# Kernel tuning notes

Hardware: AMD Instinct MI355X
Metric: run time of the kernel (lower is better)

The kernel has to match this reference:

```python
import jax, jax.numpy as jnp
import numpy as np

NUM_CLASSES = 80
ANCHORS = np.array([[10,13],[16,30],[33,23],[30,61],[62,45],[59,119],[116,90],[156,198],[373,326]], np.float32)
MASK = [[0,1,2],[3,4,5],[6,7,8]]
STRIDES = [8, 16, 32]
MAX_OUT = 100      # max_output_size_per_class == max_total_size
IOU_THR = 0.45
SCORE_THR = 0.25
NMS_TOPK = 128     # per-class candidate pre-selection for greedy NMS (>= MAX_OUT)


def setup_inputs() -> dict:
    key = jax.random.key(0)
    k1, k2, k3 = jax.random.split(key, 3)
    B = 16
    C = 3 * (NUM_CLASSES + 5)  # 255
    return {
        'p3': jax.random.normal(k1, (B, 80, 80, C), jnp.float32),
        'p4': jax.random.normal(k2, (B, 40, 40, C), jnp.float32),
        'p5': jax.random.normal(k3, (B, 20, 20, C), jnp.float32),
    }


def _decode(logits, anchors, stride):
    # logits: [B,H,W,3*(nc+5)] -> boxes [B,H*W*3,4] (x1y1x2y2), obj [B,M], cls [B,M,nc]
    B, H, W, _ = logits.shape
    A = anchors.shape[0]
    x = logits.reshape(B, H, W, A, NUM_CLASSES + 5)
    xy = jax.nn.sigmoid(x[..., :2])
    wh_logit = x[..., 2:4]
    obj = jax.nn.sigmoid(x[..., 4])
    cls = jax.nn.sigmoid(x[..., 5:])
    gx, gy = jnp.meshgrid(jnp.arange(W, dtype=x.dtype), jnp.arange(H, dtype=x.dtype))
    grid = jnp.stack([gx, gy], axis=-1)[:, :, None, :]  # [H,W,1,2]
    ctr = (xy + grid) * stride
    wh = jnp.exp(wh_logit) * anchors  # [B,H,W,A,2]
    box = jnp.concatenate([ctr - wh / 2.0, ctr + wh / 2.0], axis=-1)
    return box.reshape(B, -1, 4), obj.reshape(B, -1), cls.reshape(B, -1, NUM_CLASSES)


def _pairwise_iou(b):
    # b: [K,4] x1y1x2y2 -> [K,K]
    area = (b[:, 2] - b[:, 0]) * (b[:, 3] - b[:, 1])
    lt = jnp.maximum(b[:, None, :2], b[None, :, :2])
    rb = jnp.minimum(b[:, None, 2:], b[None, :, 2:])
    wh = jnp.clip(rb - lt, 0.0)
    inter = wh[..., 0] * wh[..., 1]
    return inter / (area[:, None] + area[None, :] - inter + 1e-9)


def _nms_single(boxes, scores):
    # boxes [N,4], scores [N] for one (image, class): greedy NMS on top-K candidates
    s = jnp.where(scores > SCORE_THR, scores, -1.0)
    top_s, idx = jax.lax.top_k(s, NMS_TOPK)   # sorted descending
    b = boxes[idx]                            # [K,4]
    iou = _pairwise_iou(b)                    # [K,K]
    rng = jnp.arange(NMS_TOPK)

    def body(keep, i):
        active = keep[i] & (top_s[i] > 0.0)
        sup = active & (iou[i] > IOU_THR) & (rng > i)
        return keep & ~sup, None

    keep, _ = jax.lax.scan(body, jnp.ones(NMS_TOPK, bool), rng)
    valid = keep & (top_s > 0.0)
    ss = jnp.where(valid, top_s, -1.0)
    sel_s, sel_i = jax.lax.top_k(ss, MAX_OUT)
    return b[sel_i], sel_s                    # [M,4], [M]


def _per_image(boxes, scores_cn):
    # boxes [N,4] shared across classes (q=1), scores_cn [C,N]
    cb, cs = jax.vmap(_nms_single, in_axes=(None, 0))(boxes, scores_cn)  # [C,M,4],[C,M]
    C = cs.shape[0]
    cls_id = jnp.broadcast_to(jnp.arange(C, dtype=boxes.dtype)[:, None], cs.shape)
    fs, fi = jax.lax.top_k(cs.reshape(-1), MAX_OUT)
    fb = cb.reshape(-1, 4)[fi]
    fc = cls_id.reshape(-1)[fi]
    valid = fs > 0.0
    n_valid = jnp.sum(valid).astype(jnp.int32)
    return (jnp.where(valid[:, None], fb, 0.0),
            jnp.where(valid, fs, 0.0),
            jnp.where(valid, fc, 0.0),
            n_valid)


def _forward(p3, p4, p5):
    boxes, objs, clss = [], [], []
    for logits, m, stride in zip((p3, p4, p5), MASK, STRIDES):
        b, o, c = _decode(logits, jnp.asarray(ANCHORS[m]), float(stride))
        boxes.append(b); objs.append(o); clss.append(c)
    boxes = jnp.concatenate(boxes, axis=1)   # [B,N,4]
    obj = jnp.concatenate(objs, axis=1)      # [B,N]
    cls = jnp.concatenate(clss, axis=1)      # [B,N,C]
    scores = obj[..., None] * cls            # [B,N,C]
    return jax.vmap(_per_image)(boxes, scores.transpose(0, 2, 1))


def reference(p3, p4, p5):
    # returns (boxes [B,100,4], scores [B,100], classes [B,100], valid [B])
    return _forward(p3, p4, p5)
```

## Files before the change

### kernel.cpp

```cpp
#include <hip/hip_runtime.h>
#include <stdint.h>

#define NUM_CLASSES 80
#define N_ANCH 25200
#define B_IMG 16
#define NMS_TOPK_ 128
#define MAX_OUT_ 100
#define SCORE_THR_ 0.25f
#define IOU_THR_ 0.45f
#define NBINS 2048
#define CAP 2048
#define CAPB 1024
#define CAPC 256
#define U8_BASE 0x3E7Eu
#define CHUNKS_PER_IMG 1575

__constant__ float c_anch[9][2] = {
    {10.f, 13.f}, {16.f, 30.f}, {33.f, 23.f},
    {30.f, 61.f}, {62.f, 45.f}, {59.f, 119.f},
    {116.f, 90.f}, {156.f, 198.f}, {373.f, 326.f}};

__device__ __forceinline__ float sigmoidf_(float x) {
    return 1.0f / (1.0f + expf(-x));
}

__device__ __forceinline__ float fast_sigmoid_(float x) {
    float t = __expf(-x);
    return __fdividef(1.0f, 1.0f + t);
}

__device__ __forceinline__ unsigned int score_u8_(float s) {
    unsigned int u = __float_as_uint(s) >> 16;
    int bin = (int)u - (int)U8_BASE;
    if (bin < 0) bin = 0;
    if (bin > 255) bin = 255;
    return (unsigned int)bin;
}

__device__ __forceinline__ unsigned int score_bin(unsigned int bits) {
    unsigned int bin = (bits - 0x3E800000u) >> 13;
    if (bin >= NBINS) bin = NBINS - 1;
    return bin;
}


__global__ void __launch_bounds__(256) decode_wave_kernel(
    const float* __restrict__ p3, const float* __restrict__ p4,
    const float* __restrict__ p5, float* __restrict__ boxes,
    unsigned char* __restrict__ score_u8) {
    int wave = threadIdx.x >> 6;
    int lane = threadIdx.x & 63;
    int chunk = blockIdx.x * 4 + wave;
    int b = chunk / CHUNKS_PER_IMG;
    int ci = chunk - b * CHUNKS_PER_IMG;
    const float* p; int W, lvl, il0, base;
    if (ci < 1200)      { p = p3; W = 80; lvl = 0; il0 = ci * 16;          base = 0;     }
    else if (ci < 1500) { p = p4; W = 40; lvl = 1; il0 = (ci - 1200) * 16; base = 19200; }
    else                { p = p5; W = 20; lvl = 2; il0 = (ci - 1500) * 16; base = 24000; }
    float stride = (float)(8 << lvl);

    __shared__ float raw_s[4][16 * 85];
    __shared__ float obj_s[4][16];
    float* raw = raw_s[wave];
    float* obj_sh = obj_s[wave];

    {
        const float4* src4 = (const float4*)(p + (size_t)b * ((size_t)W * W * 255) +
                                             (size_t)il0 * 85);
        float4* raw4 = (float4*)raw;
#pragma unroll
        for (int k = 0; k < 6; ++k) {
            int idx = lane + k * 64;
            if (idx < 340) raw4[idx] = src4[idx];
        }
    }
    __threadfence_block();

    if (lane < 16) {
        int a = lane;
        int il = il0 + a;
        int y = il / (W * 3);
        int t = il - y * (W * 3);
        int x = t / 3;
        int an = t - x * 3;
        const float* q = &raw[a * 85];
        float cx = (sigmoidf_(q[0]) + (float)x) * stride;
        float cy = (sigmoidf_(q[1]) + (float)y) * stride;
        float bw = expf(q[2]) * c_anch[lvl * 3 + an][0];
        float bh = expf(q[3]) * c_anch[lvl * 3 + an][1];
        float4 bo = {cx - bw * 0.5f, cy - bh * 0.5f,
                     cx + bw * 0.5f, cy + bh * 0.5f};
        *(float4*)(boxes + ((size_t)b * N_ANCH + base + il) * 4) = bo;
        obj_sh[a] = fast_sigmoid_(q[4]);
    }
    __threadfence_block();

    size_t rowbase = (size_t)b * NUM_CLASSES * N_ANCH + (size_t)(base + il0);
#pragma unroll
    for (int it = 0; it < 2; ++it) {
        int c = it * 64 + lane;
        if (c < NUM_CLASSES) {
            unsigned int w[4];
#pragma unroll
            for (int g = 0; g < 4; ++g) {
                unsigned int acc = 0;
#pragma unroll
                for (int a4 = 0; a4 < 4; ++a4) {
                    int a = g * 4 + a4;
                    float s = obj_sh[a] * fast_sigmoid_(raw[a * 85 + 5 + c]);
                    acc |= score_u8_(s) << (8 * a4);
                }
                w[g] = acc;
            }
            uint4 v = {w[0], w[1], w[2], w[3]};
            *(uint4*)(score_u8 + rowbase + (size_t)c * N_ANCH) = v;
        }
    }
}

__global__ void __launch_bounds__(256) select_topk_u8_kernel(
    const unsigned char* __restrict__ score_u8,
    const float* __restrict__ p3, const float* __restrict__ p4,
    const float* __restrict__ p5,
    unsigned long long* __restrict__ topsel) {
    int bc = blockIdx.x;
    int b = bc / NUM_CLASSES;
    int c = bc - b * NUM_CLASSES;
    int tid = threadIdx.x;
    int wave = tid >> 6;
    const uint4* sc = (const uint4*)(score_u8 + (size_t)bc * N_ANCH);

    __shared__ unsigned int hist[4][256];
    __shared__ unsigned long long sel[CAPB];
    __shared__ unsigned int s_cnt;
    __shared__ int s_cut;

#pragma unroll
    for (int wv = 0; wv < 4; ++wv) hist[wv][tid & 255] = 0u;
    if (tid == 0) s_cnt = 0u;
    __syncthreads();

    unsigned int* myhist = hist[wave];
    for (int i = tid; i < N_ANCH / 16; i += 256) {
        uint4 v = sc[i];
        unsigned int ww[4] = {v.x, v.y, v.z, v.w};
#pragma unroll
        for (int k = 0; k < 16; ++k) {
            unsigned int bin = (ww[k >> 2] >> ((k & 3) * 8)) & 0xFFu;
            if (bin) atomicAdd(&myhist[bin], 1u);
        }
    }
    __syncthreads();

    {
        unsigned int m = hist[0][tid] + hist[1][tid] + hist[2][tid] + hist[3][tid];
        hist[0][tid] = m;
    }
    __syncthreads();

    if (tid == 0) {
        unsigned int tot = 0; int cut = 0;
        for (int t = 255; t >= 1; --t) {
            tot += hist[0][t];
            if (tot >= NMS_TOPK_) { cut = t; break; }
        }
        s_cut = cut;
    }
    __syncthreads();
    int coll = s_cut - 1;
    if (coll < 1) coll = 1;

    for (int i = tid; i < N_ANCH / 16; i += 256) {
        uint4 v = sc[i];
        unsigned int ww[4] = {v.x, v.y, v.z, v.w};
#pragma unroll
        for (int k = 0; k < 16; ++k) {
            unsigned int bin = (ww[k >> 2] >> ((k & 3) * 8)) & 0xFFu;
            if ((int)bin >= coll) {
                unsigned int pos = atomicAdd(&s_cnt, 1u);
                if (pos < CAPB) sel[pos] = (unsigned long long)(i * 16 + k);
            }
        }
    }
    __syncthreads();

    unsigned int M = s_cnt;
    if (M > CAPB) M = CAPB;

    for (unsigned int t = tid; t < M; t += 256) {
        unsigned int idx = (unsigned int)sel[t];
        const float* q;
        if (idx < 19200u)      q = p3 + (size_t)b * 1632000 + (size_t)idx * 85;
        else if (idx < 24000u) q = p4 + (size_t)b * 408000 + (size_t)(idx - 19200u) * 85;
        else                   q = p5 + (size_t)b * 102000 + (size_t)(idx - 24000u) * 85;
        float s = sigmoidf_(q[4]) * sigmoidf_(q[5 + c]);
        sel[t] = (s > SCORE_THR_)
                     ? (((unsigned long long)__float_as_uint(s) << 32) |
                        (unsigned long long)(~idx))
                     : 0ull;
    }
    __syncthreads();

    unsigned int P2 = 1;
    while (P2 < M) P2 <<= 1;
    if (P2 < 2) P2 = 2;
    for (unsigned int k = M + tid; k < P2; k += 256) sel[k] = 0ull;
    __syncthreads();

    for (unsigned int k = 2; k <= P2; k <<= 1) {
        for (unsigned int j = k >> 1; j > 0; j >>= 1) {
            for (unsigned int t = tid; t < (int)P2; t += 256) {
                unsigned int ixj = (unsigned int)t ^ j;
                if (ixj > (unsigned int)t) {
                    unsigned long long a0 = sel[t], b0 = sel[ixj];
                    bool desc = (((unsigned int)t & k) == 0);
                    if (desc ? (a0 < b0) : (a0 > b0)) { sel[t] = b0; sel[ixj] = a0; }
                }
            }
            __syncthreads();
        }
    }

    unsigned long long* dst = topsel + (size_t)bc * NMS_TOPK_;
    if (tid < NMS_TOPK_) dst[tid] = ((unsigned int)tid < M) ? sel[tid] : 0ull;
}

__global__ void __launch_bounds__(64) nms_kernel(
    const unsigned long long* __restrict__ topsel,
    const float* __restrict__ boxes,
    float* __restrict__ cls_score, float* __restrict__ cls_box) {
    int bc = blockIdx.x;
    int b = bc / NUM_CLASSES;
    unsigned int lane = threadIdx.x;

    __shared__ float bx[NMS_TOPK_][8];

    const unsigned long long* src = topsel + (size_t)bc * NMS_TOPK_;
    unsigned long long e0 = src[lane];
    unsigned long long e1 = src[64 + lane];

    bool k0 = (e0 != 0ull);
    bool k1 = (e1 != 0ull);

    float x00 = 0, y00 = 0, x01 = 0, y01 = 0, a0 = 0, sv0 = 0;
    float x10 = 0, y10 = 0, x11 = 0, y11 = 0, a1 = 0, sv1 = 0;
    if (k0) {
        unsigned int idx = ~((unsigned int)(e0 & 0xFFFFFFFFull));
        float4 bp = *(const float4*)(boxes + ((size_t)b * N_ANCH + idx) * 4);
        x00 = bp.x; y00 = bp.y; x01 = bp.z; y01 = bp.w;
        sv0 = __uint_as_float((unsigned int)(e0 >> 32));
        a0 = (x01 - x00) * (y01 - y00);
    }
    if (k1) {
        unsigned int idx = ~((unsigned int)(e1 & 0xFFFFFFFFull));
        float4 bp = *(const float4*)(boxes + ((size_t)b * N_ANCH + idx) * 4);
        x10 = bp.x; y10 = bp.y; x11 = bp.z; y11 = bp.w;
        sv1 = __uint_as_float((unsigned int)(e1 >> 32));
        a1 = (x11 - x10) * (y11 - y10);
    }
    {
        float4 v0 = {x00, y00, x01, y01};
        float4 v1 = {x10, y10, x11, y11};
        *(float4*)&bx[lane][0] = v0;
        *(float4*)&bx[64 + lane][0] = v1;
    }
    __syncthreads();

    unsigned long long km0 = __ballot(k0);
    unsigned long long km1 = __ballot(k1);
    for (unsigned int i = 0; i < NMS_TOPK_; ++i) {
        bool ki = ((((i < 64) ? km0 : km1) >> (i & 63)) & 1ull) != 0ull;
        if (ki) {
            float4 rb = *(const float4*)&bx[i][0];
            float ra = (rb.z - rb.x) * (rb.w - rb.y);
            if (k0 && lane > i) {
                float lx = fmaxf(rb.x, x00), ly = fmaxf(rb.y, y00);
                float rx = fminf(rb.z, x01), ry = fminf(rb.w, y01);
                float w = fmaxf(rx - lx, 0.f), h = fmaxf(ry - ly, 0.f);
                float inter = w * h;
                float iou = inter / (ra + a0 - inter + 1e-9f);
                if (iou > IOU_THR_) k0 = false;
            }
            if (k1 && (64 + lane) > i) {
                float lx = fmaxf(rb.x, x10), ly = fmaxf(rb.y, y10);
                float rx = fminf(rb.z, x11), ry = fminf(rb.w, y11);
                float w = fmaxf(rx - lx, 0.f), h = fmaxf(ry - ly, 0.f);
                float inter = w * h;
                float iou = inter / (ra + a1 - inter + 1e-9f);
                if (iou > IOU_THR_) k1 = false;
            }
            km0 = __ballot(k0);
            km1 = __ballot(k1);
        }
    }

    float* scd = cls_score + (size_t)bc * MAX_OUT_;
    float* bod = cls_box + (size_t)bc * (MAX_OUT_ * 4);
    int n0 = __popcll(km0);
    int n = n0 + __popcll(km1);
    if (k0) {
        int pos = __popcll(km0 & ((1ull << lane) - 1ull));
        if (pos < MAX_OUT_) {
            scd[pos] = sv0;
            bod[pos * 4 + 0] = x00; bod[pos * 4 + 1] = y00;
            bod[pos * 4 + 2] = x01; bod[pos * 4 + 3] = y01;
        }
    }
    if (k1) {
        int pos = n0 + __popcll(km1 & ((1ull << lane) - 1ull));
        if (pos < MAX_OUT_) {
            scd[pos] = sv1;
            bod[pos * 4 + 0] = x10; bod[pos * 4 + 1] = y10;
            bod[pos * 4 + 2] = x11; bod[pos * 4 + 3] = y11;
        }
    }
    int start = n < MAX_OUT_ ? n : MAX_OUT_;
    for (int p2 = start + (int)lane; p2 < MAX_OUT_; p2 += 64) {
        scd[p2] = -1.0f;
        bod[p2 * 4 + 0] = 0.f; bod[p2 * 4 + 1] = 0.f;
        bod[p2 * 4 + 2] = 0.f; bod[p2 * 4 + 3] = 0.f;
    }
}

__global__ void __launch_bounds__(256) final_fast_kernel(
    const float* __restrict__ cls_score, const float* __restrict__ cls_box,
    float* __restrict__ out) {
    int b = blockIdx.x;
    int tid = threadIdx.x;
    const int NC = NUM_CLASSES * MAX_OUT_;
    const float* sc = cls_score + (size_t)b * NC;

    __shared__ unsigned int hist[NBINS];
    __shared__ unsigned int segsum[256];
    __shared__ unsigned long long keys[CAPC];
    __shared__ unsigned int s_cnt, s_tot;
    __shared__ int s_cut;

    for (int k = tid; k < NBINS; k += 256) hist[k] = 0u;
    if (tid == 0) s_cnt = 0u;
    __syncthreads();

    for (int k = tid; k < NC; k += 256) {
        float s = sc[k];
        if (s > 0.0f) atomicAdd(&hist[score_bin(__float_as_uint(s))], 1u);
    }
    __syncthreads();

    unsigned int ss = 0;
    for (int k = 0; k < 8; ++k) ss += hist[tid * 8 + k];
    segsum[tid] = ss;
    __syncthreads();
    if (tid == 0) {
        unsigned int total = 0;
        for (int t = 0; t < 256; ++t) total += segsum[t];
        s_tot = total;
        unsigned int tot = 0; int cut = 0; int t = 255;
        for (; t >= 0; --t) {
            if (tot + segsum[t] >= MAX_OUT_) break;
            tot += segsum[t];
        }
        if (t >= 0) {
            int j = 7;
            for (; j >= 0; --j) { tot += hist[t * 8 + j]; if (tot >= MAX_OUT_) break; }
            if (j < 0) j = 0;
            cut = t * 8 + j;
        }
        s_cut = cut;
    }
    __syncthreads();
    unsigned int cutoff = (unsigned int)s_cut;

    for (int k = tid; k < NC; k += 256) {
        float s = sc[k];
        if (s > 0.0f && score_bin(__float_as_uint(s)) >= cutoff) {
            unsigned int pos = atomicAdd(&s_cnt, 1u);
            if (pos < CAPC) {
                keys[pos] = ((unsigned long long)__float_as_uint(s) << 32) |
                            (unsigned long long)(~(unsigned int)k);
            }
        }
    }
    __syncthreads();

    unsigned int M = s_cnt;
    if (M > CAPC) M = CAPC;
    unsigned int P2 = 1;
    while (P2 < M) P2 <<= 1;
    if (P2 < 2) P2 = 2;
    for (unsigned int k = M + tid; k < P2; k += 256) keys[k] = 0ull;
    __syncthreads();

    for (unsigned int k = 2; k <= P2; k <<= 1) {
        for (unsigned int j = k >> 1; j > 0; j >>= 1) {
            for (unsigned int t = (unsigned int)tid; t < P2; t += 256) {
                unsigned int ixj = t ^ j;
                if (ixj > t) {
                    unsigned long long a0 = keys[t], b0 = keys[ixj];
                    bool desc = ((t & k) == 0);
                    if (desc ? (a0 < b0) : (a0 > b0)) { keys[t] = b0; keys[ixj] = a0; }
                }
            }
            __syncthreads();
        }
    }

    float* ob = out;
    float* os = out + B_IMG * MAX_OUT_ * 4;
    float* oc = os + B_IMG * MAX_OUT_;
    float* on = oc + B_IMG * MAX_OUT_;

    unsigned int K = M < MAX_OUT_ ? M : MAX_OUT_;
    if (tid < MAX_OUT_) {
        if ((unsigned int)tid < K) {
            unsigned long long kk = keys[tid];
            unsigned int flat = ~((unsigned int)(kk & 0xFFFFFFFFull));
            float sv = __uint_as_float((unsigned int)(kk >> 32));
            const float* bp = cls_box + ((size_t)b * NC + flat) * 4;
            os[b * MAX_OUT_ + tid] = sv;
            oc[b * MAX_OUT_ + tid] = (float)(flat / MAX_OUT_);
            ob[(b * MAX_OUT_ + tid) * 4 + 0] = bp[0];
            ob[(b * MAX_OUT_ + tid) * 4 + 1] = bp[1];
            ob[(b * MAX_OUT_ + tid) * 4 + 2] = bp[2];
            ob[(b * MAX_OUT_ + tid) * 4 + 3] = bp[3];
        } else {
            os[b * MAX_OUT_ + tid] = 0.0f;
            oc[b * MAX_OUT_ + tid] = 0.0f;
            ob[(b * MAX_OUT_ + tid) * 4 + 0] = 0.0f;
            ob[(b * MAX_OUT_ + tid) * 4 + 1] = 0.0f;
            ob[(b * MAX_OUT_ + tid) * 4 + 2] = 0.0f;
            ob[(b * MAX_OUT_ + tid) * 4 + 3] = 0.0f;
        }
    }
    if (tid == 0) {
        unsigned int nv = s_tot < MAX_OUT_ ? s_tot : MAX_OUT_;
        on[b] = (float)nv;
    }
}


__global__ void __launch_bounds__(256) decode_kernel(
    const float* __restrict__ p3, const float* __restrict__ p4,
    const float* __restrict__ p5, float* __restrict__ boxes,
    float* __restrict__ obj) {
    int gid = blockIdx.x * blockDim.x + threadIdx.x;
    if (gid >= B_IMG * N_ANCH) return;
    int b = gid / N_ANCH;
    int i = gid - b * N_ANCH;
    const float* p; int W, il, lvl; float stride;
    if (i < 19200)      { p = p3; W = 80; il = i;         lvl = 0; stride = 8.f;  }
    else if (i < 24000) { p = p4; W = 40; il = i - 19200; lvl = 1; stride = 16.f; }
    else                { p = p5; W = 20; il = i - 24000; lvl = 2; stride = 32.f; }
    int y = il / (W * 3);
    int t = il - y * W * 3;
    int x = t / 3;
    int a = t - x * 3;
    const float* q = p + ((((size_t)b * W + y) * W + x) * 255 + a * 85);
    float cx = (sigmoidf_(q[0]) + (float)x) * stride;
    float cy = (sigmoidf_(q[1]) + (float)y) * stride;
    float bw = expf(q[2]) * c_anch[lvl * 3 + a][0];
    float bh = expf(q[3]) * c_anch[lvl * 3 + a][1];
    float* bo = boxes + (size_t)gid * 4;
    bo[0] = cx - bw * 0.5f; bo[1] = cy - bh * 0.5f;
    bo[2] = cx + bw * 0.5f; bo[3] = cy + bh * 0.5f;
    obj[gid] = sigmoidf_(q[4]);
}

__device__ __forceinline__ float cand_score(
    const float* __restrict__ p3, const float* __restrict__ p4,
    const float* __restrict__ p5, const float* __restrict__ obj,
    int b, int c, int i) {
    const float* p; int W, il;
    if (i < 19200)      { p = p3; W = 80; il = i;         }
    else if (i < 24000) { p = p4; W = 40; il = i - 19200; }
    else                { p = p5; W = 20; il = i - 24000; }
    int y = il / (W * 3);
    int t = il - y * W * 3;
    int x = t / 3;
    int a = t - x * 3;
    float cl = p[(((size_t)b * W + y) * W + x) * 255 + a * 85 + 5 + c];
    return obj[b * N_ANCH + i] * sigmoidf_(cl);
}

__global__ void __launch_bounds__(256) topk_nms_kernel(
    const float* __restrict__ p3, const float* __restrict__ p4,
    const float* __restrict__ p5, const float* __restrict__ boxes,
    const float* __restrict__ obj, float* __restrict__ cls_score,
    float* __restrict__ cls_box) {
    int b = blockIdx.x / NUM_CLASSES;
    int c = blockIdx.x % NUM_CLASSES;
    int tid = threadIdx.x;

    __shared__ unsigned int hist[NBINS];
    __shared__ unsigned long long keys[CAP];
    __shared__ unsigned int s_cnt, s_cutoff;
    __shared__ float bx[NMS_TOPK_][5];
    __shared__ float bs[NMS_TOPK_];
    __shared__ int keep[NMS_TOPK_];

    for (int k = tid; k < NBINS; k += 256) hist[k] = 0u;
    if (tid == 0) s_cnt = 0u;
    __syncthreads();

    for (int i = tid; i < N_ANCH; i += 256) {
        float s = cand_score(p3, p4, p5, obj, b, c, i);
        if (s > SCORE_THR_) atomicAdd(&hist[score_bin(__float_as_uint(s))], 1u);
    }
    __syncthreads();

    if (tid == 0) {
        unsigned int total = 0;
        int cut = 0;
        for (int k = NBINS - 1; k >= 0; --k) {
            total += hist[k];
            if (total >= NMS_TOPK_) { cut = k; break; }
        }
        s_cutoff = (unsigned int)cut;
    }
    __syncthreads();
    unsigned int cutoff = s_cutoff;

    for (int i = tid; i < N_ANCH; i += 256) {
        float s = cand_score(p3, p4, p5, obj, b, c, i);
        if (s > SCORE_THR_) {
            unsigned int bits = __float_as_uint(s);
            if (score_bin(bits) >= cutoff) {
                unsigned int pos = atomicAdd(&s_cnt, 1u);
                if (pos < CAP) {
                    keys[pos] = ((unsigned long long)bits << 32) |
                                (unsigned long long)(~(unsigned int)i);
                }
            }
        }
    }
    __syncthreads();

    unsigned int M = s_cnt;
    if (M > CAP) M = CAP;
    unsigned int P2 = 1;
    while (P2 < M) P2 <<= 1;
    if (P2 < 2) P2 = 2;
    for (unsigned int k = M + tid; k < P2; k += 256) keys[k] = 0ull;
    __syncthreads();

    for (unsigned int k = 2; k <= P2; k <<= 1) {
        for (unsigned int j = k >> 1; j > 0; j >>= 1) {
            for (unsigned int t = tid; t < P2; t += 256) {
                unsigned int ixj = t ^ j;
                if (ixj > t) {
                    unsigned long long a0 = keys[t], b0 = keys[ixj];
                    bool desc = ((t & k) == 0);
                    if (desc ? (a0 < b0) : (a0 > b0)) { keys[t] = b0; keys[ixj] = a0; }
                }
            }
            __syncthreads();
        }
    }

    unsigned int K = M < NMS_TOPK_ ? M : NMS_TOPK_;
    if (tid < (int)K) {
        unsigned long long kk = keys[tid];
        unsigned int idx = ~((unsigned int)(kk & 0xFFFFFFFFull));
        const float* bp = boxes + ((size_t)b * N_ANCH + idx) * 4;
        bx[tid][0] = bp[0]; bx[tid][1] = bp[1];
        bx[tid][2] = bp[2]; bx[tid][3] = bp[3];
        bs[tid] = __uint_as_float((unsigned int)(kk >> 32));
        keep[tid] = 1;
    }
    __syncthreads();

    for (unsigned int i = 0; i < K; ++i) {
        if (keep[i]) {
            unsigned int t = (unsigned int)tid;
            if (t > i && t < K && keep[t]) {
                float ax0 = bx[i][0], ay0 = bx[i][1], ax1 = bx[i][2], ay1 = bx[i][3];
                float cx0 = bx[t][0], cy0 = bx[t][1], cx1 = bx[t][2], cy1 = bx[t][3];
                float areaA = (ax1 - ax0) * (ay1 - ay0);
                float areaB = (cx1 - cx0) * (cy1 - cy0);
                float lx = fmaxf(ax0, cx0), ly = fmaxf(ay0, cy0);
                float rx = fminf(ax1, cx1), ry = fminf(ay1, cy1);
                float w = rx - lx; if (w < 0.f) w = 0.f;
                float h = ry - ly; if (h < 0.f) h = 0.f;
                float inter = w * h;
                float iou = inter / (areaA + areaB - inter + 1e-9f);
                if (iou > IOU_THR_) keep[t] = 0;
            }
        }
        __syncthreads();
    }

    if (tid == 0) {
        float* scd = cls_score + ((size_t)b * NUM_CLASSES + c) * MAX_OUT_;
        float* bod = cls_box + ((size_t)b * NUM_CLASSES + c) * MAX_OUT_ * 4;
        int out_n = 0;
        for (unsigned int t2 = 0; t2 < K && out_n < MAX_OUT_; ++t2) {
            if (keep[t2]) {
                scd[out_n] = bs[t2];
                bod[out_n * 4 + 0] = bx[t2][0];
                bod[out_n * 4 + 1] = bx[t2][1];
                bod[out_n * 4 + 2] = bx[t2][2];
                bod[out_n * 4 + 3] = bx[t2][3];
                out_n++;
            }
        }
        for (; out_n < MAX_OUT_; ++out_n) {
            scd[out_n] = -1.0f;
            bod[out_n * 4 + 0] = 0.f; bod[out_n * 4 + 1] = 0.f;
            bod[out_n * 4 + 2] = 0.f; bod[out_n * 4 + 3] = 0.f;
        }
    }
}

extern "C" void kernel_launch(void* const* d_in, const int* in_sizes, int n_in,
                              void* d_out, int out_size, void* d_ws, size_t ws_size,
                              hipStream_t stream) {
    const float* p3 = (const float*)d_in[0];
    const float* p4 = (const float*)d_in[1];
    const float* p5 = (const float*)d_in[2];

    const size_t boxesB  = (size_t)B_IMG * N_ANCH * 4 * sizeof(float);
    const size_t clsSB   = (size_t)B_IMG * NUM_CLASSES * MAX_OUT_ * sizeof(float);
    const size_t clsBB   = clsSB * 4;
    const size_t topselB = (size_t)B_IMG * NUM_CLASSES * NMS_TOPK_ * 8;
    const size_t scoreUB = (size_t)B_IMG * NUM_CLASSES * N_ANCH;
    const size_t need_new = boxesB + clsSB + clsBB + topselB + scoreUB;

    char* base = (char*)d_ws;

    if (ws_size >= need_new) {
        float* boxes     = (float*)base;
        float* cls_score = (float*)(base + boxesB);
        float* cls_box   = (float*)(base + boxesB + clsSB);
        unsigned long long* topsel =
            (unsigned long long*)(base + boxesB + clsSB + clsBB);
        unsigned char* score_u8 =
            (unsigned char*)(base + boxesB + clsSB + clsBB + topselB);

        decode_wave_kernel<<<(B_IMG * CHUNKS_PER_IMG) / 4, 256, 0, stream>>>(
            p3, p4, p5, boxes, score_u8);
        select_topk_u8_kernel<<<B_IMG * NUM_CLASSES, 256, 0, stream>>>(
            score_u8, p3, p4, p5, topsel);
        nms_kernel<<<B_IMG * NUM_CLASSES, 64, 0, stream>>>(
            topsel, boxes, cls_score, cls_box);
        final_fast_kernel<<<B_IMG, 256, 0, stream>>>(cls_score, cls_box, (float*)d_out);
    } else {
        float* boxes = (float*)base;
        float* obj = boxes + (size_t)B_IMG * N_ANCH * 4;
        float* cls_score = obj + (size_t)B_IMG * N_ANCH;
        float* cls_box = cls_score + (size_t)B_IMG * NUM_CLASSES * MAX_OUT_;

        int tot = B_IMG * N_ANCH;
        decode_kernel<<<(tot + 255) / 256, 256, 0, stream>>>(p3, p4, p5, boxes, obj);
        topk_nms_kernel<<<B_IMG * NUM_CLASSES, 256, 0, stream>>>(
            p3, p4, p5, boxes, obj, cls_score, cls_box);
        final_fast_kernel<<<B_IMG, 256, 0, stream>>>(cls_score, cls_box, (float*)d_out);
    }
}
```

Baseline: 298.1 us.

## Decode 64-anchor tiles per block and assign classes across waves

```diff
diff --git a/kernel.cpp b/kernel.cpp
--- a/kernel.cpp
+++ b/kernel.cpp
@@ -13,7 +13,7 @@
 #define CAPB 1024
 #define CAPC 256
 #define U8_BASE 0x3E7Eu
-#define CHUNKS_PER_IMG 1575
+#define TILES_PER_IMG 394
 
 __constant__ float c_anch[9][2] = {
     {10.f, 13.f}, {16.f, 30.f}, {33.f, 23.f},
@@ -44,76 +44,63 @@
 }
 
 
-__global__ void __launch_bounds__(256) decode_wave_kernel(
+__global__ void __launch_bounds__(256) decode_tile_kernel(
     const float* __restrict__ p3, const float* __restrict__ p4,
     const float* __restrict__ p5, float* __restrict__ boxes,
     unsigned char* __restrict__ score_u8) {
-    int wave = threadIdx.x >> 6;
-    int lane = threadIdx.x & 63;
-    int chunk = blockIdx.x * 4 + wave;
-    int b = chunk / CHUNKS_PER_IMG;
-    int ci = chunk - b * CHUNKS_PER_IMG;
-    const float* p; int W, lvl, il0, base;
-    if (ci < 1200)      { p = p3; W = 80; lvl = 0; il0 = ci * 16;          base = 0;     }
-    else if (ci < 1500) { p = p4; W = 40; lvl = 1; il0 = (ci - 1200) * 16; base = 19200; }
-    else                { p = p5; W = 20; lvl = 2; il0 = (ci - 1500) * 16; base = 24000; }
+    int blk = blockIdx.x;
+    int b = blk / TILES_PER_IMG;
+    int tile = blk - b * TILES_PER_IMG;
+    const float* p; int W, lvl, il0, base, ta;
+    if (tile < 300)      { p = p3; W = 80; lvl = 0; il0 = tile * 64;         base = 0;     ta = 64; }
+    else if (tile < 375) { p = p4; W = 40; lvl = 1; il0 = (tile - 300) * 64; base = 19200; ta = 64; }
+    else                 { p = p5; W = 20; lvl = 2; il0 = (tile - 375) * 64; base = 24000;
+                           ta = (tile == 393) ? 48 : 64; }
     float stride = (float)(8 << lvl);
 
-    __shared__ float raw_s[4][16 * 85];
-    __shared__ float obj_s[4][16];
-    float* raw = raw_s[wave];
-    float* obj_sh = obj_s[wave];
+    __shared__ float raw[64 * 85];
+    int tid = threadIdx.x;
 
     {
         const float4* src4 = (const float4*)(p + (size_t)b * ((size_t)W * W * 255) +
                                              (size_t)il0 * 85);
         float4* raw4 = (float4*)raw;
+        int n4 = ta * 85 / 4;
+        for (int k = tid; k < n4; k += 256) raw4[k] = src4[k];
+    }
+    __syncthreads();
+
+    int wave = tid >> 6;
+    int lane = tid & 63;
+
+    if (lane < 16) {
+        int a = wave * 16 + lane;
+        if (a < ta) {
+            int il = il0 + a;
+            int y = il / (W * 3);
+            int t = il - y * (W * 3);
+            int x = t / 3;
+            int an = t - x * 3;
+            const float* q = &raw[a * 85];
+            float cx = (sigmoidf_(q[0]) + (float)x) * stride;
+            float cy = (sigmoidf_(q[1]) + (float)y) * stride;
+            float bw = expf(q[2]) * c_anch[lvl * 3 + an][0];
+            float bh = expf(q[3]) * c_anch[lvl * 3 + an][1];
+            float4 bo = {cx - bw * 0.5f, cy - bh * 0.5f,
+                         cx + bw * 0.5f, cy + bh * 0.5f};
+            *(float4*)(boxes + ((size_t)b * N_ANCH + base + il) * 4) = bo;
+        }
+    }
+
+    if (lane < ta) {
+        const float* q = &raw[lane * 85];
+        float obj = fast_sigmoid_(q[4]);
+        size_t sb = (size_t)b * NUM_CLASSES * N_ANCH + (size_t)(base + il0 + lane);
 #pragma unroll
-        for (int k = 0; k < 6; ++k) {
-            int idx = lane + k * 64;
-            if (idx < 340) raw4[idx] = src4[idx];
-        }
-    }
-    __threadfence_block();
-
-    if (lane < 16) {
-        int a = lane;
-        int il = il0 + a;
-        int y = il / (W * 3);
-        int t = il - y * (W * 3);
-        int x = t / 3;
-        int an = t - x * 3;
-        const float* q = &raw[a * 85];
-        float cx = (sigmoidf_(q[0]) + (float)x) * stride;
-        float cy = (sigmoidf_(q[1]) + (float)y) * stride;
-        float bw = expf(q[2]) * c_anch[lvl * 3 + an][0];
-        float bh = expf(q[3]) * c_anch[lvl * 3 + an][1];
-        float4 bo = {cx - bw * 0.5f, cy - bh * 0.5f,
-                     cx + bw * 0.5f, cy + bh * 0.5f};
-        *(float4*)(boxes + ((size_t)b * N_ANCH + base + il) * 4) = bo;
-        obj_sh[a] = fast_sigmoid_(q[4]);
-    }
-    __threadfence_block();
-
-    size_t rowbase = (size_t)b * NUM_CLASSES * N_ANCH + (size_t)(base + il0);
-#pragma unroll
-    for (int it = 0; it < 2; ++it) {
-        int c = it * 64 + lane;
-        if (c < NUM_CLASSES) {
-            unsigned int w[4];
-#pragma unroll
-            for (int g = 0; g < 4; ++g) {
-                unsigned int acc = 0;
-#pragma unroll
-                for (int a4 = 0; a4 < 4; ++a4) {
-                    int a = g * 4 + a4;
-                    float s = obj_sh[a] * fast_sigmoid_(raw[a * 85 + 5 + c]);
-                    acc |= score_u8_(s) << (8 * a4);
-                }
-                w[g] = acc;
-            }
-            uint4 v = {w[0], w[1], w[2], w[3]};
-            *(uint4*)(score_u8 + rowbase + (size_t)c * N_ANCH) = v;
+        for (int it = 0; it < 20; ++it) {
+            int c = wave * 20 + it;
+            float s = obj * fast_sigmoid_(q[5 + c]);
+            score_u8[sb + (size_t)c * N_ANCH] = (unsigned char)score_u8_(s);
         }
     }
 }
@@ -635,7 +622,7 @@
         unsigned char* score_u8 =
             (unsigned char*)(base + boxesB + clsSB + clsBB + topselB);
 
-        decode_wave_kernel<<<(B_IMG * CHUNKS_PER_IMG) / 4, 256, 0, stream>>>(
+        decode_tile_kernel<<<B_IMG * TILES_PER_IMG, 256, 0, stream>>>(
             p3, p4, p5, boxes, score_u8);
         select_topk_u8_kernel<<<B_IMG * NUM_CLASSES, 256, 0, stream>>>(
             score_u8, p3, p4, p5, topsel);
```

New measurement: 295.2 us. About the same (-1.0%).
